# Optimization experiments

Hardware: AMD Instinct MI355X
Metric: run time of the kernel (lower is better)

The kernel has to match this reference:

```python
import jax, jax.numpy as jnp
import numpy as np

B, S, H, I, E, K = 4, 1024, 1024, 768, 8, 2


def setup_inputs() -> dict:
    key = jax.random.key(0)
    ks = jax.random.split(key, 6)
    return {
        "hidden_states": jax.random.normal(ks[0], (B, S, H), dtype=jnp.float32),
        "routing_weights": jax.random.uniform(ks[1], (B, S, K), dtype=jnp.float32),
        "selected_experts": jax.random.randint(ks[2], (B, S, K), 0, E, dtype=jnp.int64),
        "gate_weight": jax.random.normal(ks[3], (E, I, H), dtype=jnp.float32) * 0.02,
        "up_weight": jax.random.normal(ks[4], (E, I, H), dtype=jnp.float32) * 0.02,
        "down_weight": jax.random.normal(ks[5], (E, H, I), dtype=jnp.float32) * 0.02,
    }


def reference(hidden_states, routing_weights, selected_experts, gate_weight, up_weight, down_weight):
    b, s, h = hidden_states.shape
    x = hidden_states.reshape(-1, h)                    # [T, H]
    T = x.shape[0]
    k = selected_experts.shape[-1]
    rw = routing_weights.astype(x.dtype).reshape(T, k)  # [T, K]
    se = selected_experts.reshape(T, k)                 # [T, K]
    e_total = gate_weight.shape[0]
    # combine[t, e] = sum of routing weights of slots of token t routed to expert e
    # (equivalent to the original per-slot dispatch + weighted scatter-add combine)
    combine = jnp.zeros((T, e_total), dtype=x.dtype).at[jnp.arange(T)[:, None], se].add(rw)
    out = jnp.zeros_like(x)
    for e in range(e_total):  # small fixed expert count
        g = x @ gate_weight[e].T                        # [T, I]
        u = x @ up_weight[e].T                          # [T, I]
        y = (jax.nn.silu(g) * u) @ down_weight[e].T     # [T, H]
        out = out + combine[:, e:e + 1] * y
    return out.reshape(b, s, h)
```

## Files before the change

kernel.cpp:

```cpp
#include <hip/hip_runtime.h>
#include <hip/hip_bf16.h>

typedef __attribute__((ext_vector_type(8))) short bf16x8;
typedef __attribute__((ext_vector_type(4))) float f32x4;

#define T_TOK 4096
#define HDIM  1024
#define IDIM  768
#define NEXP  8
#define TOPK  2
#define NSLOT (T_TOK * TOPK)

#define BM  128
#define BN  64
#define BKS 32

#define NX4 (T_TOK * HDIM / 4)
#define NW4 (NEXP * IDIM * HDIM / 4)

__device__ __forceinline__ ushort f2bf(float f) {
  union { __hip_bfloat16 h; ushort u; } cv;
  cv.h = __float2bfloat16(f);
  return cv.u;
}
__device__ __forceinline__ float bf2f(ushort u) {
  union { float f; uint v; } cv; cv.v = ((uint)u) << 16; return cv.f;
}

__device__ __forceinline__ void gload_lds16(const ushort* g, ushort* l) {
  __builtin_amdgcn_global_load_lds(
      (const __attribute__((address_space(1))) void*)g,
      (__attribute__((address_space(3))) void*)l, 16, 0, 0);
}

__global__ void cvt_all(const float* __restrict__ hs, const float* __restrict__ gw,
                        const float* __restrict__ uw, const float* __restrict__ dw,
                        ushort* __restrict__ xb, ushort* __restrict__ gwb,
                        ushort* __restrict__ uwb, ushort* __restrict__ dwb) {
  int i = blockIdx.x * blockDim.x + threadIdx.x;
  const float* src; ushort* dst; int off;
  if (i < NX4) { src = hs; dst = xb; off = i; }
  else {
    int j = i - NX4;
    if (j < NW4)            { src = gw; dst = gwb; off = j; }
    else if (j < 2 * NW4)   { src = uw; dst = uwb; off = j - NW4; }
    else                    { src = dw; dst = dwb; off = j - 2 * NW4; }
  }
  float4 v = reinterpret_cast<const float4*>(src)[off];
  ushort4 o;
  o.x = f2bf(v.x); o.y = f2bf(v.y); o.z = f2bf(v.z); o.w = f2bf(v.w);
  reinterpret_cast<ushort4*>(dst)[off] = o;
}

__global__ void route_kernel(const int* __restrict__ sel, int* __restrict__ counts,
                             int* __restrict__ toklist) {
  int slot = blockIdx.x * blockDim.x + threadIdx.x;
  if (slot >= NSLOT) return;
  int e = sel[slot];
  int idx = atomicAdd(&counts[e], 1);
  toklist[e * NSLOT + idx] = slot;
}


__launch_bounds__(256, 3)
__global__ void gemm_gateup(const ushort* __restrict__ xb,
                            const ushort* __restrict__ gwb,
                            const ushort* __restrict__ uwb,
                            const int* __restrict__ counts,
                            const int* __restrict__ toklist,
                            ushort* __restrict__ act) {
  const int b = blockIdx.x;
  const int e = b & 7;
  const int r = b >> 3;
  const int nt = r % 12, mt = r / 12;
  const int cnt = counts[e];
  const int m0 = mt * BM;
  if (m0 >= cnt) return;
  const int n0 = nt * BN;

  __shared__ __align__(16) ushort As[2][BM * BKS];
  __shared__ __align__(16) ushort Bgs[2][BN * BKS];
  __shared__ __align__(16) ushort Bus[2][BN * BKS];

  const int tid = threadIdx.x;
  const int wave = tid >> 6, lane = tid & 63;
  const int wm = wave >> 1, wn = wave & 1;
  const int lrow = lane & 15, lk16 = lane >> 4;
  const int rl = lane >> 2;
  const int gck = ((lane & 3) ^ ((lane >> 3) & 3)) << 3;

  const int ent0 = m0 + wave * 16 + rl;
  const int ent1 = ent0 + 64;
  const int arow0 = (ent0 < cnt) ? (toklist[e * NSLOT + ent0] >> 1) : 0;
  const int arow1 = (ent1 < cnt) ? (toklist[e * NSLOT + ent1] >> 1) : 0;
  const int brow = wave * 16 + rl;

  const ushort* aP0 = xb + (size_t)arow0 * HDIM + gck;
  const ushort* aP1 = xb + (size_t)arow1 * HDIM + gck;
  const ushort* gP = gwb + (size_t)e * IDIM * HDIM + (size_t)(n0 + brow) * HDIM + gck;
  const ushort* uP = uwb + (size_t)e * IDIM * HDIM + (size_t)(n0 + brow) * HDIM + gck;

  f32x4 accg[4][2], accu[4][2];
  const f32x4 fzero = {0.f, 0.f, 0.f, 0.f};
  #pragma unroll
  for (int a = 0; a < 4; ++a)
    #pragma unroll
    for (int c = 0; c < 2; ++c) { accg[a][c] = fzero; accu[a][c] = fzero; }

  auto stage = [&](int buf, int k0) {
    gload_lds16(aP0 + k0, &As[buf][wave * 512]);
    gload_lds16(aP1 + k0, &As[buf][(wave + 4) * 512]);
    gload_lds16(gP + k0, &Bgs[buf][wave * 512]);
    gload_lds16(uP + k0, &Bus[buf][wave * 512]);
  };

  const int swzc = ((lk16 ^ ((lrow >> 1) & 3)) << 3);
  auto compute = [&](int buf) {
    bf16x8 aF[4], bgF[2], buF[2];
    #pragma unroll
    for (int mi = 0; mi < 4; ++mi) {
      int rr = wm * 64 + mi * 16 + lrow;
      aF[mi] = *reinterpret_cast<const bf16x8*>(&As[buf][rr * 32 + swzc]);
    }
    #pragma unroll
    for (int ni = 0; ni < 2; ++ni) {
      int rr = wn * 32 + ni * 16 + lrow;
      bgF[ni] = *reinterpret_cast<const bf16x8*>(&Bgs[buf][rr * 32 + swzc]);
      buF[ni] = *reinterpret_cast<const bf16x8*>(&Bus[buf][rr * 32 + swzc]);
    }
    #pragma unroll
    for (int mi = 0; mi < 4; ++mi)
      #pragma unroll
      for (int ni = 0; ni < 2; ++ni) {
        accg[mi][ni] = __builtin_amdgcn_mfma_f32_16x16x32_bf16(aF[mi], bgF[ni], accg[mi][ni], 0, 0, 0);
        accu[mi][ni] = __builtin_amdgcn_mfma_f32_16x16x32_bf16(aF[mi], buF[ni], accu[mi][ni], 0, 0, 0);
      }
  };

  stage(0, 0);
  __syncthreads();
  #pragma unroll 1
  for (int t = 0; t < HDIM / BKS; t += 2) {
    if (t + 1 < HDIM / BKS) stage(1, (t + 1) * BKS);
    compute(0);
    __syncthreads();
    if (t + 2 < HDIM / BKS) stage(0, (t + 2) * BKS);
    compute(1);
    __syncthreads();
  }

  const int lcol = lane & 15;
  const int lrb = (lane >> 4) * 4;
  #pragma unroll
  for (int mi = 0; mi < 4; ++mi)
    #pragma unroll
    for (int j = 0; j < 4; ++j) {
      int row = wm * 64 + mi * 16 + lrb + j;
      int entry = m0 + row;
      if (entry >= cnt) continue;
      int slot = toklist[e * NSLOT + entry];
      #pragma unroll
      for (int ni = 0; ni < 2; ++ni) {
        int col = n0 + wn * 32 + ni * 16 + lcol;
        float g = accg[mi][ni][j];
        float u = accu[mi][ni][j];
        float y = (g / (1.0f + __expf(-g))) * u;
        act[(size_t)slot * IDIM + col] = f2bf(y);
      }
    }
}

__launch_bounds__(256, 4)
__global__ void gemm_down(const ushort* __restrict__ act,
                          const ushort* __restrict__ dwb,
                          const int* __restrict__ counts,
                          const int* __restrict__ toklist,
                          ushort* __restrict__ yact) {
  const int b = blockIdx.x;
  const int e = b & 7;
  const int r = b >> 3;
  const int nt = r & 15, mt = r >> 4;
  const int cnt = counts[e];
  const int m0 = mt * BM;
  if (m0 >= cnt) return;
  const int n0 = nt * BN;

  __shared__ __align__(16) ushort As[2][BM * BKS];
  __shared__ __align__(16) ushort Bs[2][BN * BKS];

  const int tid = threadIdx.x;
  const int wave = tid >> 6, lane = tid & 63;
  const int wm = wave >> 1, wn = wave & 1;
  const int lrow = lane & 15, lk16 = lane >> 4;
  const int rl = lane >> 2;
  const int gck = ((lane & 3) ^ ((lane >> 3) & 3)) << 3;

  const int ent0 = m0 + wave * 16 + rl;
  const int ent1 = ent0 + 64;
  const int arow0 = (ent0 < cnt) ? toklist[e * NSLOT + ent0] : 0;
  const int arow1 = (ent1 < cnt) ? toklist[e * NSLOT + ent1] : 0;
  const int brow = wave * 16 + rl;

  const ushort* aP0 = act + (size_t)arow0 * IDIM + gck;
  const ushort* aP1 = act + (size_t)arow1 * IDIM + gck;
  const ushort* dP = dwb + (size_t)e * HDIM * IDIM + (size_t)(n0 + brow) * IDIM + gck;

  f32x4 acc[4][2];
  const f32x4 fzero = {0.f, 0.f, 0.f, 0.f};
  #pragma unroll
  for (int a = 0; a < 4; ++a)
    #pragma unroll
    for (int c = 0; c < 2; ++c) acc[a][c] = fzero;

  auto stage = [&](int buf, int k0) {
    gload_lds16(aP0 + k0, &As[buf][wave * 512]);
    gload_lds16(aP1 + k0, &As[buf][(wave + 4) * 512]);
    gload_lds16(dP + k0, &Bs[buf][wave * 512]);
  };

  const int swzc = ((lk16 ^ ((lrow >> 1) & 3)) << 3);
  auto compute = [&](int buf) {
    bf16x8 aF[4], bF[2];
    #pragma unroll
    for (int mi = 0; mi < 4; ++mi) {
      int rr = wm * 64 + mi * 16 + lrow;
      aF[mi] = *reinterpret_cast<const bf16x8*>(&As[buf][rr * 32 + swzc]);
    }
    #pragma unroll
    for (int ni = 0; ni < 2; ++ni) {
      int rr = wn * 32 + ni * 16 + lrow;
      bF[ni] = *reinterpret_cast<const bf16x8*>(&Bs[buf][rr * 32 + swzc]);
    }
    #pragma unroll
    for (int mi = 0; mi < 4; ++mi)
      #pragma unroll
      for (int ni = 0; ni < 2; ++ni)
        acc[mi][ni] = __builtin_amdgcn_mfma_f32_16x16x32_bf16(aF[mi], bF[ni], acc[mi][ni], 0, 0, 0);
  };

  stage(0, 0);
  __syncthreads();
  #pragma unroll 1
  for (int t = 0; t < IDIM / BKS; t += 2) {
    if (t + 1 < IDIM / BKS) stage(1, (t + 1) * BKS);
    compute(0);
    __syncthreads();
    if (t + 2 < IDIM / BKS) stage(0, (t + 2) * BKS);
    compute(1);
    __syncthreads();
  }

  const int lcol = lane & 15;
  const int lrb = (lane >> 4) * 4;
  #pragma unroll
  for (int mi = 0; mi < 4; ++mi)
    #pragma unroll
    for (int j = 0; j < 4; ++j) {
      int row = wm * 64 + mi * 16 + lrb + j;
      int entry = m0 + row;
      if (entry >= cnt) continue;
      int slot = toklist[e * NSLOT + entry];
      #pragma unroll
      for (int ni = 0; ni < 2; ++ni) {
        int col = n0 + wn * 32 + ni * 16 + lcol;
        yact[(size_t)slot * HDIM + col] = f2bf(acc[mi][ni][j]);
      }
    }
}

__global__ void combine_kernel(const ushort* __restrict__ yact, const float* __restrict__ rw,
                               float* __restrict__ out) {
  int i = blockIdx.x * blockDim.x + threadIdx.x;
  int t = i >> 7;
  int h0 = (i & 127) << 3;
  const bf16x8 y0 = *reinterpret_cast<const bf16x8*>(yact + (size_t)(2 * t) * HDIM + h0);
  const bf16x8 y1 = *reinterpret_cast<const bf16x8*>(yact + (size_t)(2 * t + 1) * HDIM + h0);
  float w0 = rw[2 * t], w1 = rw[2 * t + 1];
  float o[8];
  #pragma unroll
  for (int j = 0; j < 8; ++j)
    o[j] = w0 * bf2f((ushort)y0[j]) + w1 * bf2f((ushort)y1[j]);
  float4* op = reinterpret_cast<float4*>(out + (size_t)t * HDIM + h0);
  op[0] = make_float4(o[0], o[1], o[2], o[3]);
  op[1] = make_float4(o[4], o[5], o[6], o[7]);
}

extern "C" void kernel_launch(void* const* d_in, const int* in_sizes, int n_in,
                              void* d_out, int out_size, void* d_ws, size_t ws_size,
                              hipStream_t stream) {
  const float* hs = (const float*)d_in[0];
  const float* rw = (const float*)d_in[1];
  const int*   se = (const int*)d_in[2];
  const float* gw = (const float*)d_in[3];
  const float* uw = (const float*)d_in[4];
  const float* dw = (const float*)d_in[5];
  float* out = (float*)d_out;

  char* base = (char*)d_ws;
  ushort* xb      = (ushort*)(base + 0);
  ushort* gwb     = (ushort*)(base + 8388608);
  ushort* uwb     = (ushort*)(base + 20971520);
  ushort* dwb     = (ushort*)(base + 33554432);
  ushort* act     = (ushort*)(base + 46137344);
  ushort* yact    = (ushort*)(base + 8388608);
  int*    toklist = (int*)(base + 58720256);
  int*    counts  = (int*)(base + 58982400);

  hipMemsetAsync(counts, 0, 256, stream);

  int total4 = NX4 + 3 * NW4;
  cvt_all<<<(total4 + 255) / 256, 256, 0, stream>>>(hs, gw, uw, dw, xb, gwb, uwb, dwb);
  route_kernel<<<NSLOT / 256, 256, 0, stream>>>(se, counts, toklist);
  gemm_gateup<<<8 * 12 * (NSLOT / BM), 256, 0, stream>>>(xb, gwb, uwb, counts, toklist, act);
  gemm_down<<<8 * 16 * (NSLOT / BM), 256, 0, stream>>>(act, dwb, counts, toklist, yact);
  combine_kernel<<<T_TOK * HDIM / 8 / 256, 256, 0, stream>>>(yact, rw, out);
}
```

Before: 237.2 us.

## Triple-buffer LDS staging with partial vmcnt waits in both expert GEMMs

Both grouped GEMM kernels switch from double to triple LDS buffering. They keep two k-tiles in flight and replace the full __syncthreads with a partial s_waitcnt vmcnt plus s_barrier, so global-to-LDS loads overlap more with MFMA compute. Buffers rotate through pointer swaps. The extra LDS use (about 48KB for gate/up) may cut occupancy under the launch bounds. Relying on vmcnt counts for correctness is fragile, and the loop has no trailing barrier before the next overwrite.

```diff
diff --git a/kernel.cpp b/kernel.cpp
--- a/kernel.cpp
+++ b/kernel.cpp
@@ -78,9 +78,9 @@
   if (m0 >= cnt) return;
   const int n0 = nt * BN;
 
-  __shared__ __align__(16) ushort As[2][BM * BKS];
-  __shared__ __align__(16) ushort Bgs[2][BN * BKS];
-  __shared__ __align__(16) ushort Bus[2][BN * BKS];
+  __shared__ __align__(16) ushort As[3][BM * BKS];
+  __shared__ __align__(16) ushort Bgs[3][BN * BKS];
+  __shared__ __align__(16) ushort Bus[3][BN * BKS];
 
   const int tid = threadIdx.x;
   const int wave = tid >> 6, lane = tid & 63;
@@ -107,26 +107,26 @@
     #pragma unroll
     for (int c = 0; c < 2; ++c) { accg[a][c] = fzero; accu[a][c] = fzero; }
 
-  auto stage = [&](int buf, int k0) {
-    gload_lds16(aP0 + k0, &As[buf][wave * 512]);
-    gload_lds16(aP1 + k0, &As[buf][(wave + 4) * 512]);
-    gload_lds16(gP + k0, &Bgs[buf][wave * 512]);
-    gload_lds16(uP + k0, &Bus[buf][wave * 512]);
+  auto stage = [&](ushort* Ab, ushort* Bgb, ushort* Bub, int k0) {
+    gload_lds16(aP0 + k0, Ab + wave * 512);
+    gload_lds16(aP1 + k0, Ab + (wave + 4) * 512);
+    gload_lds16(gP + k0, Bgb + wave * 512);
+    gload_lds16(uP + k0, Bub + wave * 512);
   };
 
   const int swzc = ((lk16 ^ ((lrow >> 1) & 3)) << 3);
-  auto compute = [&](int buf) {
+  auto compute = [&](const ushort* Ab, const ushort* Bgb, const ushort* Bub) {
     bf16x8 aF[4], bgF[2], buF[2];
     #pragma unroll
     for (int mi = 0; mi < 4; ++mi) {
       int rr = wm * 64 + mi * 16 + lrow;
-      aF[mi] = *reinterpret_cast<const bf16x8*>(&As[buf][rr * 32 + swzc]);
+      aF[mi] = *reinterpret_cast<const bf16x8*>(&Ab[rr * 32 + swzc]);
     }
     #pragma unroll
     for (int ni = 0; ni < 2; ++ni) {
       int rr = wn * 32 + ni * 16 + lrow;
-      bgF[ni] = *reinterpret_cast<const bf16x8*>(&Bgs[buf][rr * 32 + swzc]);
-      buF[ni] = *reinterpret_cast<const bf16x8*>(&Bus[buf][rr * 32 + swzc]);
+      bgF[ni] = *reinterpret_cast<const bf16x8*>(&Bgb[rr * 32 + swzc]);
+      buF[ni] = *reinterpret_cast<const bf16x8*>(&Bub[rr * 32 + swzc]);
     }
     #pragma unroll
     for (int mi = 0; mi < 4; ++mi)
@@ -137,17 +137,28 @@
       }
   };
 
-  stage(0, 0);
-  __syncthreads();
+  ushort *A0 = As[0], *A1 = As[1], *A2 = As[2];
+  ushort *G0 = Bgs[0], *G1 = Bgs[1], *G2 = Bgs[2];
+  ushort *U0 = Bus[0], *U1 = Bus[1], *U2 = Bus[2];
+
+  const int NT = HDIM / BKS;
+  stage(A0, G0, U0, 0);
+  stage(A1, G1, U1, BKS);
+
   #pragma unroll 1
-  for (int t = 0; t < HDIM / BKS; t += 2) {
-    if (t + 1 < HDIM / BKS) stage(1, (t + 1) * BKS);
-    compute(0);
-    __syncthreads();
-    if (t + 2 < HDIM / BKS) stage(0, (t + 2) * BKS);
-    compute(1);
-    __syncthreads();
+  for (int t = 0; t < NT - 1; ++t) {
+    asm volatile("s_waitcnt vmcnt(4)" ::: "memory");
+    __builtin_amdgcn_s_barrier();
+    if (t + 2 < NT) stage(A2, G2, U2, (t + 2) * BKS);
+    compute(A0, G0, U0);
+    ushort* tp;
+    tp = A0; A0 = A1; A1 = A2; A2 = tp;
+    tp = G0; G0 = G1; G1 = G2; G2 = tp;
+    tp = U0; U0 = U1; U1 = U2; U2 = tp;
   }
+  asm volatile("s_waitcnt vmcnt(0)" ::: "memory");
+  __builtin_amdgcn_s_barrier();
+  compute(A0, G0, U0);
 
   const int lcol = lane & 15;
   const int lrb = (lane >> 4) * 4;
@@ -185,8 +196,8 @@
   if (m0 >= cnt) return;
   const int n0 = nt * BN;
 
-  __shared__ __align__(16) ushort As[2][BM * BKS];
-  __shared__ __align__(16) ushort Bs[2][BN * BKS];
+  __shared__ __align__(16) ushort As[3][BM * BKS];
+  __shared__ __align__(16) ushort Bs[3][BN * BKS];
 
   const int tid = threadIdx.x;
   const int wave = tid >> 6, lane = tid & 63;
@@ -212,24 +223,24 @@
     #pragma unroll
     for (int c = 0; c < 2; ++c) acc[a][c] = fzero;
 
-  auto stage = [&](int buf, int k0) {
-    gload_lds16(aP0 + k0, &As[buf][wave * 512]);
-    gload_lds16(aP1 + k0, &As[buf][(wave + 4) * 512]);
-    gload_lds16(dP + k0, &Bs[buf][wave * 512]);
+  auto stage = [&](ushort* Ab, ushort* Bb, int k0) {
+    gload_lds16(aP0 + k0, Ab + wave * 512);
+    gload_lds16(aP1 + k0, Ab + (wave + 4) * 512);
+    gload_lds16(dP + k0, Bb + wave * 512);
   };
 
   const int swzc = ((lk16 ^ ((lrow >> 1) & 3)) << 3);
-  auto compute = [&](int buf) {
+  auto compute = [&](const ushort* Ab, const ushort* Bb) {
     bf16x8 aF[4], bF[2];
     #pragma unroll
     for (int mi = 0; mi < 4; ++mi) {
       int rr = wm * 64 + mi * 16 + lrow;
-      aF[mi] = *reinterpret_cast<const bf16x8*>(&As[buf][rr * 32 + swzc]);
+      aF[mi] = *reinterpret_cast<const bf16x8*>(&Ab[rr * 32 + swzc]);
     }
     #pragma unroll
     for (int ni = 0; ni < 2; ++ni) {
       int rr = wn * 32 + ni * 16 + lrow;
-      bF[ni] = *reinterpret_cast<const bf16x8*>(&Bs[buf][rr * 32 + swzc]);
+      bF[ni] = *reinterpret_cast<const bf16x8*>(&Bb[rr * 32 + swzc]);
     }
     #pragma unroll
     for (int mi = 0; mi < 4; ++mi)
@@ -238,17 +249,26 @@
         acc[mi][ni] = __builtin_amdgcn_mfma_f32_16x16x32_bf16(aF[mi], bF[ni], acc[mi][ni], 0, 0, 0);
   };
 
-  stage(0, 0);
-  __syncthreads();
+  ushort *A0 = As[0], *A1 = As[1], *A2 = As[2];
+  ushort *B0 = Bs[0], *B1 = Bs[1], *B2 = Bs[2];
+
+  const int NT = IDIM / BKS;
+  stage(A0, B0, 0);
+  stage(A1, B1, BKS);
+
   #pragma unroll 1
-  for (int t = 0; t < IDIM / BKS; t += 2) {
-    if (t + 1 < IDIM / BKS) stage(1, (t + 1) * BKS);
-    compute(0);
-    __syncthreads();
-    if (t + 2 < IDIM / BKS) stage(0, (t + 2) * BKS);
-    compute(1);
-    __syncthreads();
+  for (int t = 0; t < NT - 1; ++t) {
+    asm volatile("s_waitcnt vmcnt(3)" ::: "memory");
+    __builtin_amdgcn_s_barrier();
+    if (t + 2 < NT) stage(A2, B2, (t + 2) * BKS);
+    compute(A0, B0);
+    ushort* tp;
+    tp = A0; A0 = A1; A1 = A2; A2 = tp;
+    tp = B0; B0 = B1; B1 = B2; B2 = tp;
   }
+  asm volatile("s_waitcnt vmcnt(0)" ::: "memory");
+  __builtin_amdgcn_s_barrier();
+  compute(A0, B0);
 
   const int lcol = lane & 15;
   const int lrb = (lane >> 4) * 4;
```

Result: slower. 258.7 us (+9.0%).

## Widen GEMM N-tile to 128 and fuse routing into conversion kernel

Applied to the files above, without the earlier changes.

Doubles the N tile of both expert GEMMs from 64 to 128, so each wave computes a 64x64 sub-tile with twice the accumulators, which improves operand reuse from LDS and halves the grid size. Launch bounds are lowered to fit the larger register footprint. The routing pass is merged into the fp32-to-bf16 conversion kernel as 32 extra blocks, saving one kernel launch. The costs are lower occupancy and fewer blocks for load balancing across the uneven expert counts.

```diff
diff --git a/kernel.cpp b/kernel.cpp
--- a/kernel.cpp
+++ b/kernel.cpp
@@ -12,7 +12,7 @@
 #define NSLOT (T_TOK * TOPK)
 
 #define BM  128
-#define BN  64
+#define BN  128
 #define BKS 32
 
 #define NX4 (T_TOK * HDIM / 4)
@@ -33,11 +33,21 @@
       (__attribute__((address_space(3))) void*)l, 16, 0, 0);
 }
 
-__global__ void cvt_all(const float* __restrict__ hs, const float* __restrict__ gw,
-                        const float* __restrict__ uw, const float* __restrict__ dw,
-                        ushort* __restrict__ xb, ushort* __restrict__ gwb,
-                        ushort* __restrict__ uwb, ushort* __restrict__ dwb) {
-  int i = blockIdx.x * blockDim.x + threadIdx.x;
+__global__ void cvt_route(const float* __restrict__ hs, const float* __restrict__ gw,
+                          const float* __restrict__ uw, const float* __restrict__ dw,
+                          ushort* __restrict__ xb, ushort* __restrict__ gwb,
+                          ushort* __restrict__ uwb, ushort* __restrict__ dwb,
+                          const int* __restrict__ sel, int* __restrict__ counts,
+                          int* __restrict__ toklist) {
+  int bid = blockIdx.x;
+  if (bid < 32) {
+    int slot = bid * 256 + threadIdx.x;
+    int e = sel[slot];
+    int idx = atomicAdd(&counts[e], 1);
+    toklist[e * NSLOT + idx] = slot;
+    return;
+  }
+  int i = (bid - 32) * 256 + threadIdx.x;
   const float* src; ushort* dst; int off;
   if (i < NX4) { src = hs; dst = xb; off = i; }
   else {
@@ -52,17 +62,8 @@
   reinterpret_cast<ushort4*>(dst)[off] = o;
 }
 
-__global__ void route_kernel(const int* __restrict__ sel, int* __restrict__ counts,
-                             int* __restrict__ toklist) {
-  int slot = blockIdx.x * blockDim.x + threadIdx.x;
-  if (slot >= NSLOT) return;
-  int e = sel[slot];
-  int idx = atomicAdd(&counts[e], 1);
-  toklist[e * NSLOT + idx] = slot;
-}
-
-
-__launch_bounds__(256, 3)
+
+__launch_bounds__(256, 2)
 __global__ void gemm_gateup(const ushort* __restrict__ xb,
                             const ushort* __restrict__ gwb,
                             const ushort* __restrict__ uwb,
@@ -72,15 +73,15 @@
   const int b = blockIdx.x;
   const int e = b & 7;
   const int r = b >> 3;
-  const int nt = r % 12, mt = r / 12;
+  const int nt = r % 6, mt = r / 6;
   const int cnt = counts[e];
   const int m0 = mt * BM;
   if (m0 >= cnt) return;
   const int n0 = nt * BN;
 
   __shared__ __align__(16) ushort As[2][BM * BKS];
-  __shared__ __align__(16) ushort Bgs[2][BN * BKS];
-  __shared__ __align__(16) ushort Bus[2][BN * BKS];
+  __shared__ __align__(16) ushort Bgs[2][BM * BKS];
+  __shared__ __align__(16) ushort Bus[2][BM * BKS];
 
   const int tid = threadIdx.x;
   const int wave = tid >> 6, lane = tid & 63;
@@ -93,45 +94,52 @@
   const int ent1 = ent0 + 64;
   const int arow0 = (ent0 < cnt) ? (toklist[e * NSLOT + ent0] >> 1) : 0;
   const int arow1 = (ent1 < cnt) ? (toklist[e * NSLOT + ent1] >> 1) : 0;
-  const int brow = wave * 16 + rl;
+  const int brow0 = wave * 16 + rl;
+  const int brow1 = brow0 + 64;
 
   const ushort* aP0 = xb + (size_t)arow0 * HDIM + gck;
   const ushort* aP1 = xb + (size_t)arow1 * HDIM + gck;
-  const ushort* gP = gwb + (size_t)e * IDIM * HDIM + (size_t)(n0 + brow) * HDIM + gck;
-  const ushort* uP = uwb + (size_t)e * IDIM * HDIM + (size_t)(n0 + brow) * HDIM + gck;
-
-  f32x4 accg[4][2], accu[4][2];
+  const ushort* wBase = gwb + (size_t)e * IDIM * HDIM;
+  const ushort* gP0 = wBase + (size_t)(n0 + brow0) * HDIM + gck;
+  const ushort* gP1 = wBase + (size_t)(n0 + brow1) * HDIM + gck;
+  const ushort* uBase = uwb + (size_t)e * IDIM * HDIM;
+  const ushort* uP0 = uBase + (size_t)(n0 + brow0) * HDIM + gck;
+  const ushort* uP1 = uBase + (size_t)(n0 + brow1) * HDIM + gck;
+
+  f32x4 accg[4][4], accu[4][4];
   const f32x4 fzero = {0.f, 0.f, 0.f, 0.f};
   #pragma unroll
   for (int a = 0; a < 4; ++a)
     #pragma unroll
-    for (int c = 0; c < 2; ++c) { accg[a][c] = fzero; accu[a][c] = fzero; }
+    for (int c = 0; c < 4; ++c) { accg[a][c] = fzero; accu[a][c] = fzero; }
 
   auto stage = [&](int buf, int k0) {
     gload_lds16(aP0 + k0, &As[buf][wave * 512]);
     gload_lds16(aP1 + k0, &As[buf][(wave + 4) * 512]);
-    gload_lds16(gP + k0, &Bgs[buf][wave * 512]);
-    gload_lds16(uP + k0, &Bus[buf][wave * 512]);
+    gload_lds16(gP0 + k0, &Bgs[buf][wave * 512]);
+    gload_lds16(gP1 + k0, &Bgs[buf][(wave + 4) * 512]);
+    gload_lds16(uP0 + k0, &Bus[buf][wave * 512]);
+    gload_lds16(uP1 + k0, &Bus[buf][(wave + 4) * 512]);
   };
 
   const int swzc = ((lk16 ^ ((lrow >> 1) & 3)) << 3);
   auto compute = [&](int buf) {
-    bf16x8 aF[4], bgF[2], buF[2];
+    bf16x8 aF[4], bgF[4], buF[4];
     #pragma unroll
     for (int mi = 0; mi < 4; ++mi) {
       int rr = wm * 64 + mi * 16 + lrow;
       aF[mi] = *reinterpret_cast<const bf16x8*>(&As[buf][rr * 32 + swzc]);
     }
     #pragma unroll
-    for (int ni = 0; ni < 2; ++ni) {
-      int rr = wn * 32 + ni * 16 + lrow;
+    for (int ni = 0; ni < 4; ++ni) {
+      int rr = wn * 64 + ni * 16 + lrow;
       bgF[ni] = *reinterpret_cast<const bf16x8*>(&Bgs[buf][rr * 32 + swzc]);
       buF[ni] = *reinterpret_cast<const bf16x8*>(&Bus[buf][rr * 32 + swzc]);
     }
     #pragma unroll
     for (int mi = 0; mi < 4; ++mi)
       #pragma unroll
-      for (int ni = 0; ni < 2; ++ni) {
+      for (int ni = 0; ni < 4; ++ni) {
         accg[mi][ni] = __builtin_amdgcn_mfma_f32_16x16x32_bf16(aF[mi], bgF[ni], accg[mi][ni], 0, 0, 0);
         accu[mi][ni] = __builtin_amdgcn_mfma_f32_16x16x32_bf16(aF[mi], buF[ni], accu[mi][ni], 0, 0, 0);
       }
@@ -160,8 +168,8 @@
       if (entry >= cnt) continue;
       int slot = toklist[e * NSLOT + entry];
       #pragma unroll
-      for (int ni = 0; ni < 2; ++ni) {
-        int col = n0 + wn * 32 + ni * 16 + lcol;
+      for (int ni = 0; ni < 4; ++ni) {
+        int col = n0 + wn * 64 + ni * 16 + lcol;
         float g = accg[mi][ni][j];
         float u = accu[mi][ni][j];
         float y = (g / (1.0f + __expf(-g))) * u;
@@ -170,7 +178,7 @@
     }
 }
 
-__launch_bounds__(256, 4)
+__launch_bounds__(256, 3)
 __global__ void gemm_down(const ushort* __restrict__ act,
                           const ushort* __restrict__ dwb,
                           const int* __restrict__ counts,
@@ -179,14 +187,14 @@
   const int b = blockIdx.x;
   const int e = b & 7;
   const int r = b >> 3;
-  const int nt = r & 15, mt = r >> 4;
+  const int nt = r & 7, mt = r >> 3;
   const int cnt = counts[e];
   const int m0 = mt * BM;
   if (m0 >= cnt) return;
   const int n0 = nt * BN;
 
   __shared__ __align__(16) ushort As[2][BM * BKS];
-  __shared__ __align__(16) ushort Bs[2][BN * BKS];
+  __shared__ __align__(16) ushort Bs[2][BM * BKS];
 
   const int tid = threadIdx.x;
   const int wave = tid >> 6, lane = tid & 63;
@@ -199,42 +207,46 @@
   const int ent1 = ent0 + 64;
   const int arow0 = (ent0 < cnt) ? toklist[e * NSLOT + ent0] : 0;
   const int arow1 = (ent1 < cnt) ? toklist[e * NSLOT + ent1] : 0;
-  const int brow = wave * 16 + rl;
+  const int brow0 = wave * 16 + rl;
+  const int brow1 = brow0 + 64;
 
   const ushort* aP0 = act + (size_t)arow0 * IDIM + gck;
   const ushort* aP1 = act + (size_t)arow1 * IDIM + gck;
-  const ushort* dP = dwb + (size_t)e * HDIM * IDIM + (size_t)(n0 + brow) * IDIM + gck;
-
-  f32x4 acc[4][2];
+  const ushort* dBase = dwb + (size_t)e * HDIM * IDIM;
+  const ushort* dP0 = dBase + (size_t)(n0 + brow0) * IDIM + gck;
+  const ushort* dP1 = dBase + (size_t)(n0 + brow1) * IDIM + gck;
+
+  f32x4 acc[4][4];
   const f32x4 fzero = {0.f, 0.f, 0.f, 0.f};
   #pragma unroll
   for (int a = 0; a < 4; ++a)
     #pragma unroll
-    for (int c = 0; c < 2; ++c) acc[a][c] = fzero;
+    for (int c = 0; c < 4; ++c) acc[a][c] = fzero;
 
   auto stage = [&](int buf, int k0) {
     gload_lds16(aP0 + k0, &As[buf][wave * 512]);
     gload_lds16(aP1 + k0, &As[buf][(wave + 4) * 512]);
-    gload_lds16(dP + k0, &Bs[buf][wave * 512]);
+    gload_lds16(dP0 + k0, &Bs[buf][wave * 512]);
+    gload_lds16(dP1 + k0, &Bs[buf][(wave + 4) * 512]);
   };
 
   const int swzc = ((lk16 ^ ((lrow >> 1) & 3)) << 3);
   auto compute = [&](int buf) {
-    bf16x8 aF[4], bF[2];
+    bf16x8 aF[4], bF[4];
     #pragma unroll
     for (int mi = 0; mi < 4; ++mi) {
       int rr = wm * 64 + mi * 16 + lrow;
       aF[mi] = *reinterpret_cast<const bf16x8*>(&As[buf][rr * 32 + swzc]);
     }
     #pragma unroll
-    for (int ni = 0; ni < 2; ++ni) {
-      int rr = wn * 32 + ni * 16 + lrow;
+    for (int ni = 0; ni < 4; ++ni) {
+      int rr = wn * 64 + ni * 16 + lrow;
       bF[ni] = *reinterpret_cast<const bf16x8*>(&Bs[buf][rr * 32 + swzc]);
     }
     #pragma unroll
     for (int mi = 0; mi < 4; ++mi)
       #pragma unroll
-      for (int ni = 0; ni < 2; ++ni)
+      for (int ni = 0; ni < 4; ++ni)
         acc[mi][ni] = __builtin_amdgcn_mfma_f32_16x16x32_bf16(aF[mi], bF[ni], acc[mi][ni], 0, 0, 0);
   };
 
@@ -261,8 +273,8 @@
       if (entry >= cnt) continue;
       int slot = toklist[e * NSLOT + entry];
       #pragma unroll
-      for (int ni = 0; ni < 2; ++ni) {
-        int col = n0 + wn * 32 + ni * 16 + lcol;
+      for (int ni = 0; ni < 4; ++ni) {
+        int col = n0 + wn * 64 + ni * 16 + lcol;
         yact[(size_t)slot * HDIM + col] = f2bf(acc[mi][ni][j]);
       }
     }
@@ -309,9 +321,9 @@
   hipMemsetAsync(counts, 0, 256, stream);
 
   int total4 = NX4 + 3 * NW4;
-  cvt_all<<<(total4 + 255) / 256, 256, 0, stream>>>(hs, gw, uw, dw, xb, gwb, uwb, dwb);
-  route_kernel<<<NSLOT / 256, 256, 0, stream>>>(se, counts, toklist);
-  gemm_gateup<<<8 * 12 * (NSLOT / BM), 256, 0, stream>>>(xb, gwb, uwb, counts, toklist, act);
-  gemm_down<<<8 * 16 * (NSLOT / BM), 256, 0, stream>>>(act, dwb, counts, toklist, yact);
+  cvt_route<<<32 + (total4 + 255) / 256, 256, 0, stream>>>(hs, gw, uw, dw, xb, gwb, uwb, dwb,
+                                                           se, counts, toklist);
+  gemm_gateup<<<8 * 6 * (NSLOT / BM), 256, 0, stream>>>(xb, gwb, uwb, counts, toklist, act);
+  gemm_down<<<8 * 8 * (NSLOT / BM), 256, 0, stream>>>(act, dwb, counts, toklist, yact);
   combine_kernel<<<T_TOK * HDIM / 8 / 256, 256, 0, stream>>>(yact, rw, out);
 }
```

Measured after the change: 228.0 us. 3.9% less time.
